# Optimization experiments

Measured on AMD Instinct MI355X. Metric: run time of the kernel, lower is better.

## Reference

```python
import jax, jax.numpy as jnp
import numpy as np

N = 50000          # nodes
E = 1_600_000      # edges (avg degree 32)
D_IN = 128
D_OUT = 128
K = 16             # SSGC hops
ALPHA = 0.05


def setup_inputs() -> dict:
    key = jax.random.key(0)
    k1, k2, k3 = jax.random.split(key, 3)
    node_emb = jax.random.normal(k1, (N, D_IN), dtype=jnp.float32)
    edge_index = jax.random.randint(k2, (2, E), 0, N, dtype=jnp.int32)
    # Parameters of SSGConv's internal Linear(in_channels, out_channels)
    weight = jax.random.normal(k3, (D_OUT, D_IN), dtype=jnp.float32) * (1.0 / np.sqrt(D_IN))
    bias = jnp.zeros((D_OUT,), dtype=jnp.float32)
    return {"node_emb": node_emb, "edge_index": edge_index, "weight": weight, "bias": bias}


def reference(node_emb, edge_index, weight, bias):
    n = node_emb.shape[0]
    # GCN normalization with self-loops (PyG gcn_norm, add_self_loops=True)
    loops = jnp.arange(n, dtype=edge_index.dtype)
    src = jnp.concatenate([edge_index[0], loops])  # [E+N]
    dst = jnp.concatenate([edge_index[1], loops])  # [E+N]
    ones = jnp.ones(src.shape[0], dtype=node_emb.dtype)
    deg = jax.ops.segment_sum(ones, dst, num_segments=n)           # in-degree incl. self-loop
    dinv = jnp.where(deg > 0, jax.lax.rsqrt(deg), 0.0)
    norm = dinv[src] * dinv[dst]                                   # [E+N]

    def prop(x):
        msgs = norm[:, None] * x[src]                              # [E+N, D]
        return jax.ops.segment_sum(msgs, dst, num_segments=n)

    # SSGConv: h = alpha*x0 + (1-alpha)/K * sum_{k=1..K} A_hat^k x0, then Linear
    def step(carry, _):
        x, h = carry
        x = prop(x)
        h = h + ((1.0 - ALPHA) / K) * x
        return (x, h), None

    (_, h), _ = jax.lax.scan(step, (node_emb, ALPHA * node_emb), None, length=K)
    out = h @ weight.T + bias
    # Dropout(p=0.5) is identity in eval mode
    return out
```

## Files before the change

kernel.cpp:

```cpp
#include <hip/hip_runtime.h>


#define N_NODES 50000
#define N_EDGES 1600000
#define D 128
#define K_HOPS 16
#define ALPHA 0.05f
#define HCOEF ((1.0f - ALPHA) / (float)K_HOPS)

__device__ __forceinline__ unsigned int f2bf(float f) {
    unsigned int u = __float_as_uint(f);
    return (u + 0x7FFFu + ((u >> 16) & 1u)) >> 16;
}
__device__ __forceinline__ unsigned int pack_bf2(float x, float y) {
    return f2bf(x) | (f2bf(y) << 16);
}
__device__ __forceinline__ float bf_lo(unsigned int w) { return __uint_as_float(w << 16); }
__device__ __forceinline__ float bf_hi(unsigned int w) { return __uint_as_float(w & 0xFFFF0000u); }

__global__ void deg_kernel(const int* __restrict__ dst, int* __restrict__ deg,
                           int* __restrict__ rank, int e) {
    int i = blockIdx.x * blockDim.x + threadIdx.x;
    if (i < e) rank[i] = atomicAdd(&deg[dst[i]], 1);
}

__global__ void dinv_kernel(const int* __restrict__ deg, float* __restrict__ dinv,
                            float* __restrict__ selfw, int n) {
    int i = blockIdx.x * blockDim.x + threadIdx.x;
    if (i < n) {
        float di = rsqrtf((float)(deg[i] + 1));
        dinv[i] = di;
        selfw[i] = di * di;
    }
}

__global__ void scan_kernel(const int* __restrict__ deg, int* __restrict__ row_start, int n) {
    __shared__ int wsum[16];
    __shared__ int tot_s;
    __shared__ int carry_s;
    int tid = threadIdx.x, lane = tid & 63, wid = tid >> 6;
    if (tid == 0) carry_s = 0;
    __syncthreads();
    for (int base = 0; base < n; base += 1024) {
        int i = base + tid;
        int v = (i < n) ? deg[i] : 0;
        int s = v;
        #pragma unroll
        for (int off = 1; off < 64; off <<= 1) {
            int t = __shfl_up(s, off, 64);
            if (lane >= off) s += t;
        }
        if (lane == 63) wsum[wid] = s;
        __syncthreads();
        if (tid == 0) {
            int run = 0;
            #pragma unroll
            for (int w = 0; w < 16; ++w) { int t = wsum[w]; wsum[w] = run; run += t; }
            tot_s = run;
        }
        __syncthreads();
        if (i < n) row_start[i] = carry_s + wsum[wid] + (s - v);
        __syncthreads();
        if (tid == 0) carry_s += tot_s;
    }
    __syncthreads();
    if (tid == 0) row_start[n] = carry_s;
}

__global__ void scatter_kernel(const int* __restrict__ src, const int* __restrict__ dst,
                               const int* __restrict__ rank,
                               const int* __restrict__ row_start, int2* __restrict__ csr,
                               const float* __restrict__ dinv, int e) {
    int i = blockIdx.x * blockDim.x + threadIdx.x;
    if (i < e) {
        int d = dst[i];
        int s = src[i];
        int pos = row_start[d] + rank[i];
        csr[pos] = make_int2(s, __float_as_int(dinv[d] * dinv[s]));
    }
}

__global__ void init_kernel(const float2* __restrict__ x0, unsigned int* __restrict__ xb,
                            float2* __restrict__ h, int n2) {
    int i = blockIdx.x * blockDim.x + threadIdx.x;
    if (i < n2) {
        float2 v = x0[i];
        xb[i] = pack_bf2(v.x, v.y);
        h[i] = make_float2(ALPHA * v.x, ALPHA * v.y);
    }
}

#define GATHER_BLOCK(W)                                                         \
    {                                                                           \
        unsigned int g[W];                                                      \
        float wv[W];                                                            \
        _Pragma("unroll") for (int q = 0; q < W; ++q) {                         \
            int s = __shfl(rec.x, j + q);                                       \
            wv[q] = __int_as_float(__shfl(rec.y, j + q));                       \
            g[q] = xb[(size_t)s * 64 + lane];                                   \
        }                                                                       \
        _Pragma("unroll") for (int q = 0; q < W; ++q) {                         \
            accx += wv[q] * bf_lo(g[q]);                                        \
            accy += wv[q] * bf_hi(g[q]);                                        \
        }                                                                       \
        j += W;                                                                 \
    }

__global__ __launch_bounds__(256) void agg_kernel(
    const unsigned int* __restrict__ xb, unsigned int* __restrict__ yb,
    float2* __restrict__ h2, const float* __restrict__ selfw,
    const int* __restrict__ row_start, const int2* __restrict__ csr, int update_h) {
    int wid = threadIdx.x >> 6;
    int lane = threadIdx.x & 63;
    int node = blockIdx.x * 4 + wid;
    if (node >= N_NODES) return;

    int r0 = row_start[node];
    int r1 = row_start[node + 1];
    int deg = r1 - r0;
    size_t o = (size_t)node * 64 + lane;

    unsigned int vw = xb[o];
    float sw = selfw[node];
    float accx = sw * bf_lo(vw), accy = sw * bf_hi(vw);

    for (int base = 0; base < deg; base += 64) {
        int cnt = deg - base;
        if (cnt > 64) cnt = 64;
        int idx = r0 + base + lane;
        if (idx >= r1) idx = r1 - 1;
        int2 rec = csr[idx];

        int j = 0;
        while (j + 16 <= cnt) GATHER_BLOCK(16);
        if (j + 8 <= cnt) GATHER_BLOCK(8);
        if (j + 4 <= cnt) GATHER_BLOCK(4);
        for (; j < cnt; ++j) {
            int s = __shfl(rec.x, j);
            float w = __int_as_float(__shfl(rec.y, j));
            unsigned int gw = xb[(size_t)s * 64 + lane];
            accx += w * bf_lo(gw);
            accy += w * bf_hi(gw);
        }
    }

    yb[o] = pack_bf2(accx, accy);
    if (update_h) {
        float2 hv = h2[o];
        hv.x += HCOEF * (bf_lo(vw) + accx);
        hv.y += HCOEF * (bf_hi(vw) + accy);
        h2[o] = hv;
    }
}

__global__ __launch_bounds__(256) void gemm_kernel(
    const float* __restrict__ h, const float* __restrict__ w,
    const float* __restrict__ bias, float* __restrict__ out) {
    __shared__ float sAT[128][64];
    __shared__ float sBT[128][64];
    int tid = threadIdx.x;
    int row0 = blockIdx.x * 64;
    int col0 = blockIdx.y * 64;

    for (int idx = tid; idx < 64 * 32; idx += 256) {
        int r = idx & 63, kq = idx >> 6;
        float4 v;
        if (row0 + r < N_NODES)
            v = *(const float4*)&h[(size_t)(row0 + r) * D + kq * 4];
        else
            v = make_float4(0.f, 0.f, 0.f, 0.f);
        sAT[kq * 4 + 0][r] = v.x;
        sAT[kq * 4 + 1][r] = v.y;
        sAT[kq * 4 + 2][r] = v.z;
        sAT[kq * 4 + 3][r] = v.w;
    }
    for (int idx = tid; idx < 64 * 32; idx += 256) {
        int c = idx & 63, kq = idx >> 6;
        float4 v = *(const float4*)&w[(size_t)(col0 + c) * D + kq * 4];
        sBT[kq * 4 + 0][c] = v.x;
        sBT[kq * 4 + 1][c] = v.y;
        sBT[kq * 4 + 2][c] = v.z;
        sBT[kq * 4 + 3][c] = v.w;
    }
    __syncthreads();

    int cg = tid & 15;
    int rg = tid >> 4;
    float acc[4][4] = {};
    #pragma unroll 2
    for (int k = 0; k < 128; ++k) {
        float4 a = *(const float4*)&sAT[k][rg * 4];
        float4 b = *(const float4*)&sBT[k][cg * 4];
        acc[0][0] += a.x * b.x; acc[0][1] += a.x * b.y; acc[0][2] += a.x * b.z; acc[0][3] += a.x * b.w;
        acc[1][0] += a.y * b.x; acc[1][1] += a.y * b.y; acc[1][2] += a.y * b.z; acc[1][3] += a.y * b.w;
        acc[2][0] += a.z * b.x; acc[2][1] += a.z * b.y; acc[2][2] += a.z * b.z; acc[2][3] += a.z * b.w;
        acc[3][0] += a.w * b.x; acc[3][1] += a.w * b.y; acc[3][2] += a.w * b.z; acc[3][3] += a.w * b.w;
    }

    float4 bv = *(const float4*)&bias[col0 + cg * 4];
    #pragma unroll
    for (int i = 0; i < 4; ++i) {
        int r = row0 + rg * 4 + i;
        if (r < N_NODES) {
            float4 ov = make_float4(acc[i][0] + bv.x, acc[i][1] + bv.y,
                                    acc[i][2] + bv.z, acc[i][3] + bv.w);
            *(float4*)&out[(size_t)r * D + col0 + cg * 4] = ov;
        }
    }
}

extern "C" void kernel_launch(void* const* d_in, const int* in_sizes, int n_in,
                              void* d_out, int out_size, void* d_ws, size_t ws_size,
                              hipStream_t stream) {
    const float* node_emb = (const float*)d_in[0];
    const int*   edge     = (const int*)d_in[1];
    const float* weight   = (const float*)d_in[2];
    const float* bias     = (const float*)d_in[3];
    float* out = (float*)d_out;

    char* ws = (char*)d_ws;
    float*        hbuf = (float*)ws;        ws += (size_t)N_NODES * D * sizeof(float);
    unsigned int* xb0  = (unsigned int*)ws; ws += (size_t)N_NODES * 64 * sizeof(unsigned int);
    unsigned int* xb1  = (unsigned int*)ws; ws += (size_t)N_NODES * 64 * sizeof(unsigned int);
    int2*  csr      = (int2*)ws;  ws += (size_t)N_EDGES * sizeof(int2);
    int*   rank     = (int*)ws;   ws += (size_t)N_EDGES * sizeof(int);
    int*   deg      = (int*)ws;   ws += (size_t)N_NODES * sizeof(int);
    int*   row_start= (int*)ws;   ws += (size_t)(N_NODES + 1) * sizeof(int);
    float* dinv     = (float*)ws; ws += (size_t)N_NODES * sizeof(float);
    float* selfw    = (float*)ws; ws += (size_t)N_NODES * sizeof(float);

    const int* srcp = edge;
    const int* dstp = edge + N_EDGES;

    hipMemsetAsync(deg, 0, N_NODES * sizeof(int), stream);

    deg_kernel<<<(N_EDGES + 255) / 256, 256, 0, stream>>>(dstp, deg, rank, N_EDGES);
    dinv_kernel<<<(N_NODES + 255) / 256, 256, 0, stream>>>(deg, dinv, selfw, N_NODES);
    scan_kernel<<<1, 1024, 0, stream>>>(deg, row_start, N_NODES);
    scatter_kernel<<<(N_EDGES + 255) / 256, 256, 0, stream>>>(srcp, dstp, rank, row_start,
                                                              csr, dinv, N_EDGES);

    int n2 = N_NODES * D / 2;
    init_kernel<<<(n2 + 255) / 256, 256, 0, stream>>>((const float2*)node_emb, xb0,
                                                      (float2*)hbuf, n2);

    unsigned int* cur = xb0;
    unsigned int* nxt = xb1;
    for (int k = 0; k < K_HOPS; ++k) {
        agg_kernel<<<(N_NODES + 3) / 4, 256, 0, stream>>>(cur, nxt, (float2*)hbuf,
                                                          selfw, row_start, csr, k & 1);
        unsigned int* tmp = cur; cur = nxt; nxt = tmp;
    }

    dim3 ggrid((N_NODES + 63) / 64, 2);
    gemm_kernel<<<ggrid, 256, 0, stream>>>(hbuf, weight, bias, out);
}
```

Before: 1.098 ms.

## Vectorize gather to 16-byte loads, replicate degree counters, parallelize scan

The aggregation kernel now has each 16-lane group load a full 256-byte bf16 row with uint4 loads. Four neighbors are processed in parallel per wave, and a cross-group shuffle reduction combines the partial sums. Edge records are staged in LDS instead of being broadcast with shuffles. The CSR build replicates the degree counters 8 ways to reduce atomic contention and replaces the single-block scan with a three-pass multi-block scan. The cost is the extra reduction shuffles and extra per-edge replica-offset lookups.

Result: slower. 1.157 ms (+5.4%).

```diff
diff --git a/kernel.cpp b/kernel.cpp
--- a/kernel.cpp
+++ b/kernel.cpp
@@ -7,6 +7,8 @@
 #define K_HOPS 16
 #define ALPHA 0.05f
 #define HCOEF ((1.0f - ALPHA) / (float)K_HOPS)
+#define NREP 8
+#define N_SBLK ((N_NODES + 255) / 256)
 
 __device__ __forceinline__ unsigned int f2bf(float f) {
     unsigned int u = __float_as_uint(f);
@@ -18,64 +20,88 @@
 __device__ __forceinline__ float bf_lo(unsigned int w) { return __uint_as_float(w << 16); }
 __device__ __forceinline__ float bf_hi(unsigned int w) { return __uint_as_float(w & 0xFFFF0000u); }
 
-__global__ void deg_kernel(const int* __restrict__ dst, int* __restrict__ deg,
+__global__ void deg_kernel(const int* __restrict__ dst, int* __restrict__ degR,
                            int* __restrict__ rank, int e) {
-    int i = blockIdx.x * blockDim.x + threadIdx.x;
-    if (i < e) rank[i] = atomicAdd(&deg[dst[i]], 1);
-}
-
-__global__ void dinv_kernel(const int* __restrict__ deg, float* __restrict__ dinv,
-                            float* __restrict__ selfw, int n) {
-    int i = blockIdx.x * blockDim.x + threadIdx.x;
+    int i = blockIdx.x * 256 + threadIdx.x;
+    if (i < e) {
+        int rep = blockIdx.x & (NREP - 1);
+        rank[i] = atomicAdd(&degR[rep * N_NODES + dst[i]], 1);
+    }
+}
+
+__global__ void combine_kernel(int* __restrict__ degR, int* __restrict__ deg,
+                               float* __restrict__ dinv, float* __restrict__ selfw, int n) {
+    int i = blockIdx.x * 256 + threadIdx.x;
     if (i < n) {
-        float di = rsqrtf((float)(deg[i] + 1));
+        int run = 0;
+        #pragma unroll
+        for (int r = 0; r < NREP; ++r) {
+            int v = degR[r * N_NODES + i];
+            degR[r * N_NODES + i] = run;
+            run += v;
+        }
+        deg[i] = run;
+        float di = rsqrtf((float)(run + 1));
         dinv[i] = di;
         selfw[i] = di * di;
     }
 }
 
-__global__ void scan_kernel(const int* __restrict__ deg, int* __restrict__ row_start, int n) {
-    __shared__ int wsum[16];
-    __shared__ int tot_s;
-    __shared__ int carry_s;
+__device__ __forceinline__ int block_scan_excl(int v) {
+    __shared__ int ws[4];
     int tid = threadIdx.x, lane = tid & 63, wid = tid >> 6;
-    if (tid == 0) carry_s = 0;
+    int s = v;
+    #pragma unroll
+    for (int off = 1; off < 64; off <<= 1) {
+        int t = __shfl_up(s, off, 64);
+        if (lane >= off) s += t;
+    }
+    if (lane == 63) ws[wid] = s;
     __syncthreads();
-    for (int base = 0; base < n; base += 1024) {
-        int i = base + tid;
-        int v = (i < n) ? deg[i] : 0;
-        int s = v;
-        #pragma unroll
-        for (int off = 1; off < 64; off <<= 1) {
-            int t = __shfl_up(s, off, 64);
-            if (lane >= off) s += t;
-        }
-        if (lane == 63) wsum[wid] = s;
-        __syncthreads();
-        if (tid == 0) {
-            int run = 0;
-            #pragma unroll
-            for (int w = 0; w < 16; ++w) { int t = wsum[w]; wsum[w] = run; run += t; }
-            tot_s = run;
-        }
-        __syncthreads();
-        if (i < n) row_start[i] = carry_s + wsum[wid] + (s - v);
-        __syncthreads();
-        if (tid == 0) carry_s += tot_s;
-    }
+    int woff = 0;
+    #pragma unroll
+    for (int w = 0; w < 3; ++w)
+        if (w < wid) woff += ws[w];
+    return woff + s - v;
+}
+
+__global__ void scan_part(const int* __restrict__ deg, int* __restrict__ part, int n) {
+    int i = blockIdx.x * 256 + threadIdx.x;
+    int v = (i < n) ? deg[i] : 0;
+    #pragma unroll
+    for (int off = 1; off < 64; off <<= 1) v += __shfl_xor(v, off, 64);
+    __shared__ int ws[4];
+    if ((threadIdx.x & 63) == 0) ws[threadIdx.x >> 6] = v;
     __syncthreads();
-    if (tid == 0) row_start[n] = carry_s;
+    if (threadIdx.x == 0) part[blockIdx.x] = ws[0] + ws[1] + ws[2] + ws[3];
+}
+
+__global__ void scan_mid(int* __restrict__ part, int nb) {
+    int tid = threadIdx.x;
+    int v = (tid < nb) ? part[tid] : 0;
+    int e = block_scan_excl(v);
+    if (tid < nb) part[tid] = e;
+}
+
+__global__ void scan_fin(const int* __restrict__ deg, const int* __restrict__ part,
+                         int* __restrict__ row_start, int n) {
+    int i = blockIdx.x * 256 + threadIdx.x;
+    int v = (i < n) ? deg[i] : 0;
+    int e = block_scan_excl(v) + part[blockIdx.x];
+    if (i < n) row_start[i] = e;
+    if (i == n - 1) row_start[n] = e + v;
 }
 
 __global__ void scatter_kernel(const int* __restrict__ src, const int* __restrict__ dst,
-                               const int* __restrict__ rank,
-                               const int* __restrict__ row_start, int2* __restrict__ csr,
+                               const int* __restrict__ rank, const int* __restrict__ row_start,
+                               const int* __restrict__ pref, int2* __restrict__ csr,
                                const float* __restrict__ dinv, int e) {
-    int i = blockIdx.x * blockDim.x + threadIdx.x;
+    int i = blockIdx.x * 256 + threadIdx.x;
     if (i < e) {
+        int rep = blockIdx.x & (NREP - 1);
         int d = dst[i];
         int s = src[i];
-        int pos = row_start[d] + rank[i];
+        int pos = row_start[d] + pref[rep * N_NODES + d] + rank[i];
         csr[pos] = make_int2(s, __float_as_int(dinv[d] * dinv[s]));
     }
 }
@@ -90,66 +116,93 @@
     }
 }
 
-#define GATHER_BLOCK(W)                                                         \
-    {                                                                           \
-        unsigned int g[W];                                                      \
-        float wv[W];                                                            \
-        _Pragma("unroll") for (int q = 0; q < W; ++q) {                         \
-            int s = __shfl(rec.x, j + q);                                       \
-            wv[q] = __int_as_float(__shfl(rec.y, j + q));                       \
-            g[q] = xb[(size_t)s * 64 + lane];                                   \
-        }                                                                       \
-        _Pragma("unroll") for (int q = 0; q < W; ++q) {                         \
-            accx += wv[q] * bf_lo(g[q]);                                        \
-            accy += wv[q] * bf_hi(g[q]);                                        \
-        }                                                                       \
-        j += W;                                                                 \
+#define ACC8(W, G)                                                          \
+    acc[0] += (W) * bf_lo((G).x); acc[1] += (W) * bf_hi((G).x);             \
+    acc[2] += (W) * bf_lo((G).y); acc[3] += (W) * bf_hi((G).y);             \
+    acc[4] += (W) * bf_lo((G).z); acc[5] += (W) * bf_hi((G).z);             \
+    acc[6] += (W) * bf_lo((G).w); acc[7] += (W) * bf_hi((G).w);
+
+#define GATHER_STEP(NW)                                                     \
+    {                                                                       \
+        int2 er[NW];                                                        \
+        uint4 gr[NW];                                                       \
+        _Pragma("unroll") for (int q = 0; q < (NW); ++q)                    \
+            er[q] = srec[wid][j + 4 * q + grp];                             \
+        _Pragma("unroll") for (int q = 0; q < (NW); ++q)                    \
+            gr[q] = xb4[(er[q].x << 4) + sub];                              \
+        _Pragma("unroll") for (int q = 0; q < (NW); ++q) {                  \
+            float w = __int_as_float(er[q].y);                              \
+            ACC8(w, gr[q]);                                                 \
+        }                                                                   \
+        j += 4 * (NW);                                                      \
     }
 
 __global__ __launch_bounds__(256) void agg_kernel(
-    const unsigned int* __restrict__ xb, unsigned int* __restrict__ yb,
-    float2* __restrict__ h2, const float* __restrict__ selfw,
+    const uint4* __restrict__ xb4, uint4* __restrict__ yb4,
+    float4* __restrict__ h4, const float* __restrict__ selfw,
     const int* __restrict__ row_start, const int2* __restrict__ csr, int update_h) {
+    __shared__ int2 srec[4][64];
     int wid = threadIdx.x >> 6;
     int lane = threadIdx.x & 63;
+    int grp = lane >> 4, sub = lane & 15;
     int node = blockIdx.x * 4 + wid;
     if (node >= N_NODES) return;
 
     int r0 = row_start[node];
     int r1 = row_start[node + 1];
-    int deg = r1 - r0;
-    size_t o = (size_t)node * 64 + lane;
-
-    unsigned int vw = xb[o];
-    float sw = selfw[node];
-    float accx = sw * bf_lo(vw), accy = sw * bf_hi(vw);
-
-    for (int base = 0; base < deg; base += 64) {
-        int cnt = deg - base;
+    int dg = r1 - r0;
+
+    float acc[8] = {0.f, 0.f, 0.f, 0.f, 0.f, 0.f, 0.f, 0.f};
+
+    for (int base = 0; base < dg; base += 64) {
+        int cnt = dg - base;
         if (cnt > 64) cnt = 64;
         int idx = r0 + base + lane;
         if (idx >= r1) idx = r1 - 1;
-        int2 rec = csr[idx];
+        srec[wid][lane] = csr[idx];
 
         int j = 0;
-        while (j + 16 <= cnt) GATHER_BLOCK(16);
-        if (j + 8 <= cnt) GATHER_BLOCK(8);
-        if (j + 4 <= cnt) GATHER_BLOCK(4);
-        for (; j < cnt; ++j) {
-            int s = __shfl(rec.x, j);
-            float w = __int_as_float(__shfl(rec.y, j));
-            unsigned int gw = xb[(size_t)s * 64 + lane];
-            accx += w * bf_lo(gw);
-            accy += w * bf_hi(gw);
+        while (j + 32 <= cnt) GATHER_STEP(8);
+        while (j + 16 <= cnt) GATHER_STEP(4);
+        if (j + 8 <= cnt) GATHER_STEP(2);
+        while (j < cnt) {
+            int2 er = srec[wid][j + grp];
+            uint4 gr = xb4[(er.x << 4) + sub];
+            float w = (j + grp < cnt) ? __int_as_float(er.y) : 0.f;
+            ACC8(w, gr);
+            j += 4;
         }
     }
 
-    yb[o] = pack_bf2(accx, accy);
-    if (update_h) {
-        float2 hv = h2[o];
-        hv.x += HCOEF * (bf_lo(vw) + accx);
-        hv.y += HCOEF * (bf_hi(vw) + accy);
-        h2[o] = hv;
+    #pragma unroll
+    for (int q = 0; q < 8; ++q) {
+        acc[q] += __shfl_xor(acc[q], 16, 64);
+        acc[q] += __shfl_xor(acc[q], 32, 64);
+    }
+
+    if (grp == 0) {
+        int o = (node << 4) + sub;
+        uint4 vw = xb4[o];
+        float sw = selfw[node];
+        float xs[8] = {bf_lo(vw.x), bf_hi(vw.x), bf_lo(vw.y), bf_hi(vw.y),
+                       bf_lo(vw.z), bf_hi(vw.z), bf_lo(vw.w), bf_hi(vw.w)};
+        #pragma unroll
+        for (int q = 0; q < 8; ++q) acc[q] += sw * xs[q];
+        uint4 ov;
+        ov.x = pack_bf2(acc[0], acc[1]);
+        ov.y = pack_bf2(acc[2], acc[3]);
+        ov.z = pack_bf2(acc[4], acc[5]);
+        ov.w = pack_bf2(acc[6], acc[7]);
+        yb4[o] = ov;
+        if (update_h) {
+            int ho = (node << 5) + (sub << 1);
+            float4 h0 = h4[ho], h1 = h4[ho + 1];
+            h0.x += HCOEF * (xs[0] + acc[0]); h0.y += HCOEF * (xs[1] + acc[1]);
+            h0.z += HCOEF * (xs[2] + acc[2]); h0.w += HCOEF * (xs[3] + acc[3]);
+            h1.x += HCOEF * (xs[4] + acc[4]); h1.y += HCOEF * (xs[5] + acc[5]);
+            h1.z += HCOEF * (xs[6] + acc[6]); h1.w += HCOEF * (xs[7] + acc[7]);
+            h4[ho] = h0; h4[ho + 1] = h1;
+        }
     }
 }
 
@@ -224,21 +277,25 @@
     unsigned int* xb1  = (unsigned int*)ws; ws += (size_t)N_NODES * 64 * sizeof(unsigned int);
     int2*  csr      = (int2*)ws;  ws += (size_t)N_EDGES * sizeof(int2);
     int*   rank     = (int*)ws;   ws += (size_t)N_EDGES * sizeof(int);
+    int*   degR     = (int*)ws;   ws += (size_t)NREP * N_NODES * sizeof(int);
     int*   deg      = (int*)ws;   ws += (size_t)N_NODES * sizeof(int);
-    int*   row_start= (int*)ws;   ws += (size_t)(N_NODES + 1) * sizeof(int);
+    int*   row_start= (int*)ws;   ws += (size_t)(N_NODES + 16) * sizeof(int);
     float* dinv     = (float*)ws; ws += (size_t)N_NODES * sizeof(float);
     float* selfw    = (float*)ws; ws += (size_t)N_NODES * sizeof(float);
+    int*   part     = (int*)ws;   ws += 256 * sizeof(int);
 
     const int* srcp = edge;
     const int* dstp = edge + N_EDGES;
 
-    hipMemsetAsync(deg, 0, N_NODES * sizeof(int), stream);
-
-    deg_kernel<<<(N_EDGES + 255) / 256, 256, 0, stream>>>(dstp, deg, rank, N_EDGES);
-    dinv_kernel<<<(N_NODES + 255) / 256, 256, 0, stream>>>(deg, dinv, selfw, N_NODES);
-    scan_kernel<<<1, 1024, 0, stream>>>(deg, row_start, N_NODES);
+    hipMemsetAsync(degR, 0, (size_t)NREP * N_NODES * sizeof(int), stream);
+
+    deg_kernel<<<(N_EDGES + 255) / 256, 256, 0, stream>>>(dstp, degR, rank, N_EDGES);
+    combine_kernel<<<(N_NODES + 255) / 256, 256, 0, stream>>>(degR, deg, dinv, selfw, N_NODES);
+    scan_part<<<N_SBLK, 256, 0, stream>>>(deg, part, N_NODES);
+    scan_mid<<<1, 256, 0, stream>>>(part, N_SBLK);
+    scan_fin<<<N_SBLK, 256, 0, stream>>>(deg, part, row_start, N_NODES);
     scatter_kernel<<<(N_EDGES + 255) / 256, 256, 0, stream>>>(srcp, dstp, rank, row_start,
-                                                              csr, dinv, N_EDGES);
+                                                              degR, csr, dinv, N_EDGES);
 
     int n2 = N_NODES * D / 2;
     init_kernel<<<(n2 + 255) / 256, 256, 0, stream>>>((const float2*)node_emb, xb0,
@@ -247,8 +304,8 @@
     unsigned int* cur = xb0;
     unsigned int* nxt = xb1;
     for (int k = 0; k < K_HOPS; ++k) {
-        agg_kernel<<<(N_NODES + 3) / 4, 256, 0, stream>>>(cur, nxt, (float2*)hbuf,
-                                                          selfw, row_start, csr, k & 1);
+        agg_kernel<<<(N_NODES + 3) / 4, 256, 0, stream>>>(
+            (const uint4*)cur, (uint4*)nxt, (float4*)hbuf, selfw, row_start, csr, k & 1);
         unsigned int* tmp = cur; cur = nxt; nxt = tmp;
     }
 
```

## Replicate degree counters, parallelize CSR prefix scan, vectorize scatter

Applied to the files above, without the earlier changes.

Degree counting now spreads atomics over 8 replicated counter arrays chosen by edge-index chunk, which cuts contention on hot nodes, and each thread handles 8 edges with vector loads. A combine kernel folds the replicas into per-replica prefix offsets plus the total degree and dinv. The single-block serial scan is replaced by a three-phase multi-block scan. The scatter processes 4 edges per thread and adds the replica offset when computing positions. This targets the CSR build preprocessing, which is small next to the 16 aggregation hops, and it adds extra kernel launches and extra memory for the replicas.

New measurement: 1.072 ms. 1.02x faster.

```diff
diff --git a/kernel.cpp b/kernel.cpp
--- a/kernel.cpp
+++ b/kernel.cpp
@@ -7,6 +7,11 @@
 #define K_HOPS 16
 #define ALPHA 0.05f
 #define HCOEF ((1.0f - ALPHA) / (float)K_HOPS)
+#define NREP 8
+#define N_SBLK ((N_NODES + 255) / 256)
+
+#define DEG_IPT 8
+#define REP_OF(i) (((i) >> 11) & (NREP - 1))
 
 __device__ __forceinline__ unsigned int f2bf(float f) {
     unsigned int u = __float_as_uint(f);
@@ -18,66 +23,115 @@
 __device__ __forceinline__ float bf_lo(unsigned int w) { return __uint_as_float(w << 16); }
 __device__ __forceinline__ float bf_hi(unsigned int w) { return __uint_as_float(w & 0xFFFF0000u); }
 
-__global__ void deg_kernel(const int* __restrict__ dst, int* __restrict__ deg,
+__global__ void deg_kernel(const int* __restrict__ dst, int* __restrict__ degR,
                            int* __restrict__ rank, int e) {
-    int i = blockIdx.x * blockDim.x + threadIdx.x;
-    if (i < e) rank[i] = atomicAdd(&deg[dst[i]], 1);
-}
-
-__global__ void dinv_kernel(const int* __restrict__ deg, float* __restrict__ dinv,
-                            float* __restrict__ selfw, int n) {
-    int i = blockIdx.x * blockDim.x + threadIdx.x;
+    int gid = blockIdx.x * 256 + threadIdx.x;
+    int i0 = gid * DEG_IPT;
+    if (i0 >= e) return;
+    int rep = REP_OF(i0);
+    int* base = degR + rep * N_NODES;
+    int4 d0 = *(const int4*)&dst[i0];
+    int4 d1 = *(const int4*)&dst[i0 + 4];
+    int r[8];
+    r[0] = atomicAdd(&base[d0.x], 1);
+    r[1] = atomicAdd(&base[d0.y], 1);
+    r[2] = atomicAdd(&base[d0.z], 1);
+    r[3] = atomicAdd(&base[d0.w], 1);
+    r[4] = atomicAdd(&base[d1.x], 1);
+    r[5] = atomicAdd(&base[d1.y], 1);
+    r[6] = atomicAdd(&base[d1.z], 1);
+    r[7] = atomicAdd(&base[d1.w], 1);
+    *(int4*)&rank[i0]     = make_int4(r[0], r[1], r[2], r[3]);
+    *(int4*)&rank[i0 + 4] = make_int4(r[4], r[5], r[6], r[7]);
+}
+
+__global__ void combine_kernel(int* __restrict__ degR, int* __restrict__ deg,
+                               float* __restrict__ dinv, float* __restrict__ selfw, int n) {
+    int i = blockIdx.x * 256 + threadIdx.x;
     if (i < n) {
-        float di = rsqrtf((float)(deg[i] + 1));
+        int run = 0;
+        #pragma unroll
+        for (int r = 0; r < NREP; ++r) {
+            int v = degR[r * N_NODES + i];
+            degR[r * N_NODES + i] = run;
+            run += v;
+        }
+        deg[i] = run;
+        float di = rsqrtf((float)(run + 1));
         dinv[i] = di;
         selfw[i] = di * di;
     }
 }
 
-__global__ void scan_kernel(const int* __restrict__ deg, int* __restrict__ row_start, int n) {
-    __shared__ int wsum[16];
-    __shared__ int tot_s;
-    __shared__ int carry_s;
+__device__ __forceinline__ int block_scan_excl(int v) {
+    __shared__ int ws[4];
     int tid = threadIdx.x, lane = tid & 63, wid = tid >> 6;
-    if (tid == 0) carry_s = 0;
+    int s = v;
+    #pragma unroll
+    for (int off = 1; off < 64; off <<= 1) {
+        int t = __shfl_up(s, off, 64);
+        if (lane >= off) s += t;
+    }
+    if (lane == 63) ws[wid] = s;
     __syncthreads();
-    for (int base = 0; base < n; base += 1024) {
-        int i = base + tid;
-        int v = (i < n) ? deg[i] : 0;
-        int s = v;
-        #pragma unroll
-        for (int off = 1; off < 64; off <<= 1) {
-            int t = __shfl_up(s, off, 64);
-            if (lane >= off) s += t;
-        }
-        if (lane == 63) wsum[wid] = s;
-        __syncthreads();
-        if (tid == 0) {
-            int run = 0;
-            #pragma unroll
-            for (int w = 0; w < 16; ++w) { int t = wsum[w]; wsum[w] = run; run += t; }
-            tot_s = run;
-        }
-        __syncthreads();
-        if (i < n) row_start[i] = carry_s + wsum[wid] + (s - v);
-        __syncthreads();
-        if (tid == 0) carry_s += tot_s;
-    }
+    int woff = 0;
+    #pragma unroll
+    for (int w = 0; w < 3; ++w)
+        if (w < wid) woff += ws[w];
+    return woff + s - v;
+}
+
+__global__ void scan_part(const int* __restrict__ deg, int* __restrict__ part, int n) {
+    int i = blockIdx.x * 256 + threadIdx.x;
+    int v = (i < n) ? deg[i] : 0;
+    #pragma unroll
+    for (int off = 1; off < 64; off <<= 1) v += __shfl_xor(v, off, 64);
+    __shared__ int ws[4];
+    if ((threadIdx.x & 63) == 0) ws[threadIdx.x >> 6] = v;
     __syncthreads();
-    if (tid == 0) row_start[n] = carry_s;
+    if (threadIdx.x == 0) part[blockIdx.x] = ws[0] + ws[1] + ws[2] + ws[3];
+}
+
+__global__ void scan_mid(int* __restrict__ part, int nb) {
+    int tid = threadIdx.x;
+    int v = (tid < nb) ? part[tid] : 0;
+    int e = block_scan_excl(v);
+    if (tid < nb) part[tid] = e;
+}
+
+__global__ void scan_fin(const int* __restrict__ deg, const int* __restrict__ part,
+                         int* __restrict__ row_start, int n) {
+    int i = blockIdx.x * 256 + threadIdx.x;
+    int v = (i < n) ? deg[i] : 0;
+    int e = block_scan_excl(v) + part[blockIdx.x];
+    if (i < n) row_start[i] = e;
+    if (i == n - 1) row_start[n] = e + v;
 }
 
 __global__ void scatter_kernel(const int* __restrict__ src, const int* __restrict__ dst,
-                               const int* __restrict__ rank,
-                               const int* __restrict__ row_start, int2* __restrict__ csr,
+                               const int* __restrict__ rank, const int* __restrict__ row_start,
+                               const int* __restrict__ pref, int2* __restrict__ csr,
                                const float* __restrict__ dinv, int e) {
-    int i = blockIdx.x * blockDim.x + threadIdx.x;
-    if (i < e) {
-        int d = dst[i];
-        int s = src[i];
-        int pos = row_start[d] + rank[i];
-        csr[pos] = make_int2(s, __float_as_int(dinv[d] * dinv[s]));
-    }
+    int gid = blockIdx.x * 256 + threadIdx.x;
+    int i0 = gid * 4;
+    if (i0 >= e) return;
+    int4 dv = *(const int4*)&dst[i0];
+    int4 sv = *(const int4*)&src[i0];
+    int4 rv = *(const int4*)&rank[i0];
+    int d[4] = {dv.x, dv.y, dv.z, dv.w};
+    int s[4] = {sv.x, sv.y, sv.z, sv.w};
+    int r[4] = {rv.x, rv.y, rv.z, rv.w};
+    int pos[4];
+    float w[4];
+    #pragma unroll
+    for (int q = 0; q < 4; ++q) {
+        int rep = REP_OF(i0 + q);
+        pos[q] = row_start[d[q]] + pref[rep * N_NODES + d[q]] + r[q];
+        w[q] = dinv[d[q]] * dinv[s[q]];
+    }
+    #pragma unroll
+    for (int q = 0; q < 4; ++q)
+        csr[pos[q]] = make_int2(s[q], __float_as_int(w[q]));
 }
 
 __global__ void init_kernel(const float2* __restrict__ x0, unsigned int* __restrict__ xb,
@@ -224,21 +278,27 @@
     unsigned int* xb1  = (unsigned int*)ws; ws += (size_t)N_NODES * 64 * sizeof(unsigned int);
     int2*  csr      = (int2*)ws;  ws += (size_t)N_EDGES * sizeof(int2);
     int*   rank     = (int*)ws;   ws += (size_t)N_EDGES * sizeof(int);
+    int*   degR     = (int*)ws;   ws += (size_t)NREP * N_NODES * sizeof(int);
     int*   deg      = (int*)ws;   ws += (size_t)N_NODES * sizeof(int);
-    int*   row_start= (int*)ws;   ws += (size_t)(N_NODES + 1) * sizeof(int);
+    int*   row_start= (int*)ws;   ws += (size_t)(N_NODES + 16) * sizeof(int);
     float* dinv     = (float*)ws; ws += (size_t)N_NODES * sizeof(float);
     float* selfw    = (float*)ws; ws += (size_t)N_NODES * sizeof(float);
+    int*   part     = (int*)ws;   ws += 256 * sizeof(int);
 
     const int* srcp = edge;
     const int* dstp = edge + N_EDGES;
 
-    hipMemsetAsync(deg, 0, N_NODES * sizeof(int), stream);
-
-    deg_kernel<<<(N_EDGES + 255) / 256, 256, 0, stream>>>(dstp, deg, rank, N_EDGES);
-    dinv_kernel<<<(N_NODES + 255) / 256, 256, 0, stream>>>(deg, dinv, selfw, N_NODES);
-    scan_kernel<<<1, 1024, 0, stream>>>(deg, row_start, N_NODES);
-    scatter_kernel<<<(N_EDGES + 255) / 256, 256, 0, stream>>>(srcp, dstp, rank, row_start,
-                                                              csr, dinv, N_EDGES);
+    hipMemsetAsync(degR, 0, (size_t)NREP * N_NODES * sizeof(int), stream);
+
+    int deg_threads = N_EDGES / DEG_IPT;
+    deg_kernel<<<(deg_threads + 255) / 256, 256, 0, stream>>>(dstp, degR, rank, N_EDGES);
+    combine_kernel<<<(N_NODES + 255) / 256, 256, 0, stream>>>(degR, deg, dinv, selfw, N_NODES);
+    scan_part<<<N_SBLK, 256, 0, stream>>>(deg, part, N_NODES);
+    scan_mid<<<1, 256, 0, stream>>>(part, N_SBLK);
+    scan_fin<<<N_SBLK, 256, 0, stream>>>(deg, part, row_start, N_NODES);
+    int sc_threads = N_EDGES / 4;
+    scatter_kernel<<<(sc_threads + 255) / 256, 256, 0, stream>>>(srcp, dstp, rank, row_start,
+                                                                 degR, csr, dinv, N_EDGES);
 
     int n2 = N_NODES * D / 2;
     init_kernel<<<(n2 + 255) / 256, 256, 0, stream>>>((const float2*)node_emb, xb0,
```
